# Performance work log

Measured on AMD Instinct MI355X. Metric: run time of the kernel, lower is better.

The kernel has to match this reference:

```python
import jax, jax.numpy as jnp
import numpy as np

K_SAMPLES = 1024   # number of farthest-point samples (self.K)
K_NEIGH = 64       # neighbors per ball (self.k_classes)
RADIUS = 0.2       # ball-query radius
LAYERS = [64, 64, 128]
IN_CH = 3


def _fps_indices(pts, k):
    """Iterative farthest point sampling (pytorch3d-style, start at index 0).
    pts: (B, N, D) -> idx: (B, k) int32."""
    B, N, D = pts.shape
    big = jnp.asarray(1e10, pts.dtype)

    def step(carry, _):
        min_d, last = carry                                   # (B,N), (B,)
        lp = jnp.take_along_axis(pts, last[:, None, None], axis=1)  # (B,1,D)
        d = jnp.sum((pts - lp) ** 2, axis=-1)                 # (B,N)
        min_d = jnp.minimum(min_d, d)
        nxt = jnp.argmax(min_d, axis=-1).astype(jnp.int32)    # farthest so far
        return (min_d, nxt), nxt

    init = (jnp.full((B, N), big, pts.dtype), jnp.zeros((B,), jnp.int32))
    _, rest = jax.lax.scan(step, init, None, length=k - 1)    # (k-1, B)
    idx = jnp.concatenate([jnp.zeros((1, B), jnp.int32), rest], axis=0)
    return idx.T                                              # (B, k)


def _ball_query(queries, pts, k, radius):
    """For each query take the first k points of pts within radius (by index
    order, as in pytorch3d.ball_query); pad missing neighbors with zeros.
    queries: (B,K,D), pts: (B,N,D) -> grouped: (B,K,k,D)."""
    B, N, D = pts.shape
    q2 = jnp.sum(queries ** 2, axis=-1)                       # (B,K)
    p2 = jnp.sum(pts ** 2, axis=-1)                           # (B,N)
    d2 = q2[:, :, None] + p2[:, None, :] - 2.0 * jnp.einsum('bkd,bnd->bkn', queries, pts)
    valid = d2 < radius * radius                              # (B,K,N)
    arange_n = jnp.arange(N, dtype=jnp.int32)
    key = jnp.where(valid, arange_n, N)                       # invalid -> sentinel N
    neg_vals, nbr_idx = jax.lax.top_k(-key, k)                # k smallest keys
    taken_valid = (-neg_vals) < N                             # (B,K,k)
    grouped = jax.vmap(lambda p, i: p[i])(pts, nbr_idx)       # (B,K,k,D)
    grouped = jnp.where(taken_valid[..., None], grouped, jnp.zeros((), pts.dtype))
    return grouped


def setup_inputs() -> dict:
    key = jax.random.key(0)
    ks = jax.random.split(key, 7)
    points = jax.random.uniform(ks[0], (8, 4096, IN_CH), dtype=jnp.float32)
    dims = [IN_CH] + LAYERS
    inp = {'points': points}
    for li in range(len(LAYERS)):
        fan_in = dims[li]
        w = jax.random.normal(ks[1 + li], (dims[li], dims[li + 1]), dtype=jnp.float32) / np.sqrt(fan_in)
        b = jnp.zeros((dims[li + 1],), jnp.float32)
        inp[f'w{li}'] = w
        inp[f'b{li}'] = b
    return inp


def reference(points, w0, b0, w1, b1, w2, b2):
    # 1) farthest point sampling of K centroids
    fps_idx = _fps_indices(points, K_SAMPLES)                 # (B,K)
    selected = jax.vmap(lambda p, i: p[i])(points, fps_idx)   # (B,K,C)
    selected_xyz = selected[:, :, :3]
    # 2) ball query grouping around the centroids
    grouped = _ball_query(selected, points, K_NEIGH, RADIUS)  # (B,K,k,C)
    # 3) shared PointNet MLP (pointwise 1x1 conv == linear) + max-pool over neighbors
    h = grouped
    for w, b in ((w0, b0), (w1, b1), (w2, b2)):
        h = jax.nn.relu(jnp.einsum('bknc,cd->bknd', h, w) + b)
    feat = jnp.max(h, axis=2)                                 # (B,K,layers[-1])
    # 4) concat centroid xyz with pooled features
    return jnp.concatenate([selected_xyz, feat], axis=2)      # (B,K,3+128)
```

## Files before the change

kernel.cpp:

```cpp
#include <hip/hip_runtime.h>

#define BATCH 8
#define NPTS 4096
#define KSAMP 1024
#define KNEI 64
#define OUTC 131

__device__ __forceinline__ unsigned long long umax64(unsigned long long a,
                                                     unsigned long long b)
{
    return a > b ? a : b;
}

#define DPP_U64_STEP(v, CTRL)                                                  \
    {                                                                          \
        int _lo = __builtin_amdgcn_update_dpp(0, (int)(unsigned)(v), (CTRL),   \
                                              0xF, 0xF, true);                 \
        int _hi = __builtin_amdgcn_update_dpp(0, (int)((v) >> 32), (CTRL),     \
                                              0xF, 0xF, true);                 \
        unsigned long long _o =                                                \
            ((unsigned long long)(unsigned)_hi << 32) | (unsigned)_lo;         \
        (v) = umax64((v), _o);                                                 \
    }

__device__ __forceinline__ unsigned long long wave_umax64(unsigned long long v)
{
    DPP_U64_STEP(v, 0x111)
    DPP_U64_STEP(v, 0x112)
    DPP_U64_STEP(v, 0x114)
    DPP_U64_STEP(v, 0x118)
    DPP_U64_STEP(v, 0x142)
    DPP_U64_STEP(v, 0x143)
    return v;
}

#define DPP_F32MAX_STEP(v, CTRL)                                               \
    {                                                                          \
        int _s = __builtin_amdgcn_update_dpp(0, __float_as_int(v), (CTRL),     \
                                             0xF, 0xF, true);                  \
        (v) = fmaxf((v), __int_as_float(_s));                                  \
    }

__device__ __forceinline__ float wave_fmax_nonneg(float v)
{
    DPP_F32MAX_STEP(v, 0x111)
    DPP_F32MAX_STEP(v, 0x112)
    DPP_F32MAX_STEP(v, 0x114)
    DPP_F32MAX_STEP(v, 0x118)
    DPP_F32MAX_STEP(v, 0x142)
    DPP_F32MAX_STEP(v, 0x143)
    return v;
}

#define FPS_T 256
#define FPS_PPT 16

__global__ __launch_bounds__(FPS_T) void fps_kernel(const float* __restrict__ pts,
                                                    float* __restrict__ out)
{
    const int b = blockIdx.x;
    const int t = threadIdx.x;
    const float* p = pts + (size_t)b * NPTS * 3;

    __shared__ float lx[NPTS], ly[NPTS], lz[NPTS];
    __shared__ unsigned long long cand[2][4];

    float px[FPS_PPT], py[FPS_PPT], pz[FPS_PPT], md[FPS_PPT];
#pragma unroll
    for (int i = 0; i < FPS_PPT; ++i) {
        const int n = t * FPS_PPT + i;
        px[i] = p[n * 3 + 0];
        py[i] = p[n * 3 + 1];
        pz[i] = p[n * 3 + 2];
        lx[n] = px[i]; ly[n] = py[i]; lz[n] = pz[i];
        md[i] = 1e10f;
    }
    if (t == 0) {
        float* o = out + (size_t)b * KSAMP * OUTC;
        o[0] = p[0]; o[1] = p[1]; o[2] = p[2];
    }
    __syncthreads();

    const int wave = t >> 6;
    const int lane = t & 63;
    int cur = 0;

    for (int s = 1; s < KSAMP; ++s) {
        const float qx = lx[cur], qy = ly[cur], qz = lz[cur];

#pragma unroll
        for (int i = 0; i < FPS_PPT; ++i) {
            float dx = px[i] - qx, dy = py[i] - qy, dz = pz[i] - qz;
            float d = dx * dx + dy * dy + dz * dz;
            md[i] = fminf(md[i], d);
        }

        unsigned long long c[FPS_PPT];
#pragma unroll
        for (int i = 0; i < FPS_PPT; ++i)
            c[i] = ((unsigned long long)__float_as_uint(md[i]) << 32)
                 | (unsigned)(4095 - (t * FPS_PPT + i));
#pragma unroll
        for (int i = 0; i < 8; ++i) c[i] = umax64(c[i], c[i + 8]);
#pragma unroll
        for (int i = 0; i < 4; ++i) c[i] = umax64(c[i], c[i + 4]);
        c[0] = umax64(c[0], c[2]);
        c[1] = umax64(c[1], c[3]);
        unsigned long long best = umax64(c[0], c[1]);

        best = wave_umax64(best);
        const int par = s & 1;
        if (lane == 63) cand[par][wave] = best;
        __syncthreads();

        unsigned long long g = umax64(umax64(cand[par][0], cand[par][1]),
                                      umax64(cand[par][2], cand[par][3]));
        cur = 4095 - (int)(g & 0xffffffffu);

        if (t == 0) {
            float* o = out + ((size_t)b * KSAMP + s) * OUTC;
            o[0] = lx[cur]; o[1] = ly[cur]; o[2] = lz[cur];
        }
    }
}

__global__ __launch_bounds__(64) void bqmlp_kernel(
    const float* __restrict__ pts,
    const float* __restrict__ w0, const float* __restrict__ b0,
    const float* __restrict__ w1, const float* __restrict__ b1,
    const float* __restrict__ w2, const float* __restrict__ b2,
    float* __restrict__ out)
{
    const int q    = blockIdx.x;
    const int b    = q >> 10;
    const int lane = threadIdx.x;
    const float* p = pts + (size_t)b * NPTS * 3;
    float* orow    = out + (size_t)q * OUTC;

    const float qx = orow[0], qy = orow[1], qz = orow[2];

    const float RR = 0.04f;
    const float q2 = __fadd_rn(__fadd_rn(__fmul_rn(qx, qx), __fmul_rn(qy, qy)),
                               __fmul_rn(qz, qz));

    __shared__ float nx[KNEI], ny[KNEI], nz[KNEI];
    nx[lane] = 0.0f; ny[lane] = 0.0f; nz[lane] = 0.0f;
    __syncthreads();

    int total = 0;
    for (int c = 0; c < NPTS / 64 && total < KNEI; ++c) {
        const int n = c * 64 + lane;
        const float x = p[n * 3 + 0];
        const float y = p[n * 3 + 1];
        const float z = p[n * 3 + 2];
        const float p2  = __fadd_rn(__fadd_rn(__fmul_rn(x, x), __fmul_rn(y, y)),
                                    __fmul_rn(z, z));
        const float dot = __fadd_rn(__fadd_rn(__fmul_rn(qx, x), __fmul_rn(qy, y)),
                                    __fmul_rn(qz, z));
        const float d2  = __fsub_rn(__fadd_rn(q2, p2), __fmul_rn(2.0f, dot));
        const bool valid = d2 < RR;
        const unsigned long long mask = __ballot(valid);
        const int pos = total + (int)__popcll(mask & ((1ull << lane) - 1ull));
        if (valid && pos < KNEI) { nx[pos] = x; ny[pos] = y; nz[pos] = z; }
        total += (int)__popcll(mask);
    }
    __syncthreads();

    const float x = nx[lane], y = ny[lane], z = nz[lane];

    float h0[64];
#pragma unroll
    for (int j = 0; j < 64; ++j) {
        float a = fmaf(x, w0[j], fmaf(y, w0[64 + j], fmaf(z, w0[128 + j], b0[j])));
        h0[j] = fmaxf(a, 0.0f);
    }

    float h1[64];
#pragma unroll
    for (int jb = 0; jb < 4; ++jb) {
        float acc[16];
#pragma unroll
        for (int i = 0; i < 16; ++i) acc[i] = b1[jb * 16 + i];
#pragma unroll
        for (int k = 0; k < 64; ++k) {
#pragma unroll
            for (int i = 0; i < 16; ++i)
                acc[i] = fmaf(h0[k], w1[k * 64 + jb * 16 + i], acc[i]);
        }
#pragma unroll
        for (int i = 0; i < 16; ++i) h1[jb * 16 + i] = fmaxf(acc[i], 0.0f);
    }

#pragma unroll
    for (int jb = 0; jb < 8; ++jb) {
        float acc[16];
#pragma unroll
        for (int i = 0; i < 16; ++i) acc[i] = b2[jb * 16 + i];
#pragma unroll
        for (int k = 0; k < 64; ++k) {
#pragma unroll
            for (int i = 0; i < 16; ++i)
                acc[i] = fmaf(h1[k], w2[k * 128 + jb * 16 + i], acc[i]);
        }
#pragma unroll
        for (int i = 0; i < 16; ++i) {
            float v = fmaxf(acc[i], 0.0f);
            acc[i] = wave_fmax_nonneg(v);
        }
        if (lane == 63) {
#pragma unroll
            for (int i = 0; i < 16; ++i) orow[3 + jb * 16 + i] = acc[i];
        }
    }
}

extern "C" void kernel_launch(void* const* d_in, const int* in_sizes, int n_in,
                              void* d_out, int out_size, void* d_ws, size_t ws_size,
                              hipStream_t stream)
{
    (void)in_sizes; (void)n_in; (void)out_size; (void)d_ws; (void)ws_size;
    const float* pts = (const float*)d_in[0];
    const float* w0  = (const float*)d_in[1];
    const float* b0  = (const float*)d_in[2];
    const float* w1  = (const float*)d_in[3];
    const float* b1  = (const float*)d_in[4];
    const float* w2  = (const float*)d_in[5];
    const float* b2  = (const float*)d_in[6];
    float* out = (float*)d_out;

    hipLaunchKernelGGL(fps_kernel, dim3(BATCH), dim3(FPS_T), 0, stream, pts, out);
    hipLaunchKernelGGL(bqmlp_kernel, dim3(BATCH * KSAMP), dim3(64), 0, stream,
                       pts, w0, b0, w1, b1, w2, b2, out);
}
```

Baseline: 974.1 us.

## Pack FPS distance math, use index-tracked argmax, stage MLP weights in LDS

The FPS loop now computes distances with packed v_pk FP32 instructions and runs its per-thread argmax as float compares with index selects, building only one 64-bit key before the wave reduction. It also loads the next query point right after the reduction. The ball-query/MLP kernel now runs four queries per 256-thread block and stages all weights and biases in LDS as float4, in place of scalar global loads per lane. The LDS cost is about 50KB per block, which may limit occupancy, and staging adds a block-wide barrier.

```diff
diff --git a/kernel.cpp b/kernel.cpp
--- a/kernel.cpp
+++ b/kernel.cpp
@@ -5,6 +5,19 @@
 #define KSAMP 1024
 #define KNEI 64
 #define OUTC 131
+
+typedef float v2f __attribute__((ext_vector_type(2)));
+typedef float v4f __attribute__((ext_vector_type(4)));
+
+__device__ __forceinline__ v2f pk_add(v2f a, v2f b) {
+    v2f d; asm("v_pk_add_f32 %0, %1, %2" : "=v"(d) : "v"(a), "v"(b)); return d;
+}
+__device__ __forceinline__ v2f pk_mul(v2f a, v2f b) {
+    v2f d; asm("v_pk_mul_f32 %0, %1, %2" : "=v"(d) : "v"(a), "v"(b)); return d;
+}
+__device__ __forceinline__ v2f pk_fma(v2f a, v2f b, v2f c) {
+    v2f d; asm("v_pk_fma_f32 %0, %1, %2, %3" : "=v"(d) : "v"(a), "v"(b), "v"(c)); return d;
+}
 
 __device__ __forceinline__ unsigned long long umax64(unsigned long long a,
                                                      unsigned long long b)
@@ -65,15 +78,20 @@
     __shared__ float lx[NPTS], ly[NPTS], lz[NPTS];
     __shared__ unsigned long long cand[2][4];
 
-    float px[FPS_PPT], py[FPS_PPT], pz[FPS_PPT], md[FPS_PPT];
+    v2f pxp[8], pyp[8], pzp[8], mdp[8];
+    int idxr[16];
 #pragma unroll
     for (int i = 0; i < FPS_PPT; ++i) {
         const int n = t * FPS_PPT + i;
-        px[i] = p[n * 3 + 0];
-        py[i] = p[n * 3 + 1];
-        pz[i] = p[n * 3 + 2];
-        lx[n] = px[i]; ly[n] = py[i]; lz[n] = pz[i];
-        md[i] = 1e10f;
+        const float x = p[n * 3 + 0];
+        const float y = p[n * 3 + 1];
+        const float z = p[n * 3 + 2];
+        pxp[i >> 1][i & 1] = x;
+        pyp[i >> 1][i & 1] = y;
+        pzp[i >> 1][i & 1] = z;
+        mdp[i >> 1][i & 1] = 1e10f;
+        lx[n] = x; ly[n] = y; lz[n] = z;
+        idxr[i] = n;
     }
     if (t == 0) {
         float* o = out + (size_t)b * KSAMP * OUTC;
@@ -83,69 +101,111 @@
 
     const int wave = t >> 6;
     const int lane = t & 63;
-    int cur = 0;
+    float qx = lx[0], qy = ly[0], qz = lz[0];
+
+#define MD(i) ((i) & 1 ? mdp[(i) >> 1].y : mdp[(i) >> 1].x)
 
     for (int s = 1; s < KSAMP; ++s) {
-        const float qx = lx[cur], qy = ly[cur], qz = lz[cur];
-
-#pragma unroll
-        for (int i = 0; i < FPS_PPT; ++i) {
-            float dx = px[i] - qx, dy = py[i] - qy, dz = pz[i] - qz;
-            float d = dx * dx + dy * dy + dz * dz;
-            md[i] = fminf(md[i], d);
-        }
-
-        unsigned long long c[FPS_PPT];
-#pragma unroll
-        for (int i = 0; i < FPS_PPT; ++i)
-            c[i] = ((unsigned long long)__float_as_uint(md[i]) << 32)
-                 | (unsigned)(4095 - (t * FPS_PPT + i));
-#pragma unroll
-        for (int i = 0; i < 8; ++i) c[i] = umax64(c[i], c[i + 8]);
-#pragma unroll
-        for (int i = 0; i < 4; ++i) c[i] = umax64(c[i], c[i + 4]);
-        c[0] = umax64(c[0], c[2]);
-        c[1] = umax64(c[1], c[3]);
-        unsigned long long best = umax64(c[0], c[1]);
-
-        best = wave_umax64(best);
+        const float nqx = -qx, nqy = -qy, nqz = -qz;
+        const v2f nqx2 = {nqx, nqx}, nqy2 = {nqy, nqy}, nqz2 = {nqz, nqz};
+
+#pragma unroll
+        for (int j = 0; j < 8; ++j) {
+            v2f dx = pk_add(pxp[j], nqx2);
+            v2f dy = pk_add(pyp[j], nqy2);
+            v2f dz = pk_add(pzp[j], nqz2);
+            v2f d  = pk_fma(dz, dz, pk_fma(dy, dy, pk_mul(dx, dx)));
+            mdp[j].x = fminf(mdp[j].x, d.x);
+            mdp[j].y = fminf(mdp[j].y, d.y);
+        }
+
+        float tv[8]; int ti[8];
+#pragma unroll
+        for (int i = 0; i < 8; ++i) {
+            const float a = MD(i), c = MD(i + 8);
+            const bool g = c > a;
+            tv[i] = g ? c : a;
+            ti[i] = g ? idxr[i + 8] : idxr[i];
+        }
+#pragma unroll
+        for (int i = 0; i < 4; ++i) {
+            const bool g = tv[i + 4] > tv[i];
+            tv[i] = g ? tv[i + 4] : tv[i];
+            ti[i] = g ? ti[i + 4] : ti[i];
+        }
+#pragma unroll
+        for (int i = 0; i < 2; ++i) {
+            const bool g = tv[i + 2] > tv[i];
+            tv[i] = g ? tv[i + 2] : tv[i];
+            ti[i] = g ? ti[i + 2] : ti[i];
+        }
+        const bool g0 = tv[1] > tv[0];
+        const float bv = g0 ? tv[1] : tv[0];
+        const int   bi = g0 ? ti[1] : ti[0];
+
+        unsigned long long key =
+            ((unsigned long long)__float_as_uint(bv) << 32) | (unsigned)(4095 - bi);
+        key = wave_umax64(key);
         const int par = s & 1;
-        if (lane == 63) cand[par][wave] = best;
+        if (lane == 63) cand[par][wave] = key;
         __syncthreads();
 
-        unsigned long long g = umax64(umax64(cand[par][0], cand[par][1]),
-                                      umax64(cand[par][2], cand[par][3]));
-        cur = 4095 - (int)(g & 0xffffffffu);
-
+        const unsigned long long g =
+            umax64(umax64(cand[par][0], cand[par][1]),
+                   umax64(cand[par][2], cand[par][3]));
+        const int cur = 4095 - (int)(g & 0xffffffffu);
+
+        qx = lx[cur]; qy = ly[cur]; qz = lz[cur];
         if (t == 0) {
             float* o = out + ((size_t)b * KSAMP + s) * OUTC;
-            o[0] = lx[cur]; o[1] = ly[cur]; o[2] = lz[cur];
-        }
-    }
-}
-
-__global__ __launch_bounds__(64) void bqmlp_kernel(
+            o[0] = qx; o[1] = qy; o[2] = qz;
+        }
+    }
+#undef MD
+}
+
+__global__ __launch_bounds__(256, 3) void bqmlp_kernel(
     const float* __restrict__ pts,
     const float* __restrict__ w0, const float* __restrict__ b0,
     const float* __restrict__ w1, const float* __restrict__ b1,
     const float* __restrict__ w2, const float* __restrict__ b2,
     float* __restrict__ out)
 {
-    const int q    = blockIdx.x;
-    const int b    = q >> 10;
-    const int lane = threadIdx.x;
-    const float* p = pts + (size_t)b * NPTS * 3;
+    const int t    = threadIdx.x;
+    const int wv   = t >> 6;
+    const int lane = t & 63;
+    const int q    = blockIdx.x * 4 + wv;
+    const int bb   = q >> 10;
+    const float* p = pts + (size_t)bb * NPTS * 3;
     float* orow    = out + (size_t)q * OUTC;
 
+    __shared__ v4f sw0[48];
+    __shared__ v4f sb0[16];
+    __shared__ v4f sw1[1024];
+    __shared__ v4f sb1[16];
+    __shared__ v4f sw2[2048];
+    __shared__ v4f sb2[32];
+    __shared__ float snx[4][KNEI], sny[4][KNEI], snz[4][KNEI];
+
+    {
+        const v4f* g1 = (const v4f*)w1;
+#pragma unroll
+        for (int i = 0; i < 4; ++i) sw1[t + i * 256] = g1[t + i * 256];
+        const v4f* g2 = (const v4f*)w2;
+#pragma unroll
+        for (int i = 0; i < 8; ++i) sw2[t + i * 256] = g2[t + i * 256];
+        if (t < 48) sw0[t] = ((const v4f*)w0)[t];
+        if (t < 16) sb0[t] = ((const v4f*)b0)[t];
+        if (t < 16) sb1[t] = ((const v4f*)b1)[t];
+        if (t < 32) sb2[t] = ((const v4f*)b2)[t];
+    }
+
     const float qx = orow[0], qy = orow[1], qz = orow[2];
-
     const float RR = 0.04f;
     const float q2 = __fadd_rn(__fadd_rn(__fmul_rn(qx, qx), __fmul_rn(qy, qy)),
                                __fmul_rn(qz, qz));
 
-    __shared__ float nx[KNEI], ny[KNEI], nz[KNEI];
-    nx[lane] = 0.0f; ny[lane] = 0.0f; nz[lane] = 0.0f;
-    __syncthreads();
+    snx[wv][lane] = 0.0f; sny[wv][lane] = 0.0f; snz[wv][lane] = 0.0f;
 
     int total = 0;
     for (int c = 0; c < NPTS / 64 && total < KNEI; ++c) {
@@ -161,18 +221,23 @@
         const bool valid = d2 < RR;
         const unsigned long long mask = __ballot(valid);
         const int pos = total + (int)__popcll(mask & ((1ull << lane) - 1ull));
-        if (valid && pos < KNEI) { nx[pos] = x; ny[pos] = y; nz[pos] = z; }
+        if (valid && pos < KNEI) { snx[wv][pos] = x; sny[wv][pos] = y; snz[wv][pos] = z; }
         total += (int)__popcll(mask);
     }
+
     __syncthreads();
 
-    const float x = nx[lane], y = ny[lane], z = nz[lane];
+    const float x = snx[wv][lane], y = sny[wv][lane], z = snz[wv][lane];
 
     float h0[64];
 #pragma unroll
-    for (int j = 0; j < 64; ++j) {
-        float a = fmaf(x, w0[j], fmaf(y, w0[64 + j], fmaf(z, w0[128 + j], b0[j])));
-        h0[j] = fmaxf(a, 0.0f);
+    for (int j4 = 0; j4 < 16; ++j4) {
+        const v4f wx = sw0[j4], wy = sw0[16 + j4], wz = sw0[32 + j4], bv = sb0[j4];
+#pragma unroll
+        for (int c = 0; c < 4; ++c) {
+            float a = fmaf(x, wx[c], fmaf(y, wy[c], fmaf(z, wz[c], bv[c])));
+            h0[j4 * 4 + c] = fmaxf(a, 0.0f);
+        }
     }
 
     float h1[64];
@@ -180,12 +245,25 @@
     for (int jb = 0; jb < 4; ++jb) {
         float acc[16];
 #pragma unroll
-        for (int i = 0; i < 16; ++i) acc[i] = b1[jb * 16 + i];
+        for (int i4 = 0; i4 < 4; ++i4) {
+            const v4f bv = sb1[jb * 4 + i4];
+#pragma unroll
+            for (int c = 0; c < 4; ++c) acc[i4 * 4 + c] = bv[c];
+        }
 #pragma unroll
         for (int k = 0; k < 64; ++k) {
-#pragma unroll
-            for (int i = 0; i < 16; ++i)
-                acc[i] = fmaf(h0[k], w1[k * 64 + jb * 16 + i], acc[i]);
+            const float hk = h0[k];
+            const v4f wA = sw1[k * 16 + jb * 4 + 0];
+            const v4f wB = sw1[k * 16 + jb * 4 + 1];
+            const v4f wC = sw1[k * 16 + jb * 4 + 2];
+            const v4f wD = sw1[k * 16 + jb * 4 + 3];
+#pragma unroll
+            for (int c = 0; c < 4; ++c) {
+                acc[c]      = fmaf(hk, wA[c], acc[c]);
+                acc[4 + c]  = fmaf(hk, wB[c], acc[4 + c]);
+                acc[8 + c]  = fmaf(hk, wC[c], acc[8 + c]);
+                acc[12 + c] = fmaf(hk, wD[c], acc[12 + c]);
+            }
         }
 #pragma unroll
         for (int i = 0; i < 16; ++i) h1[jb * 16 + i] = fmaxf(acc[i], 0.0f);
@@ -195,12 +273,25 @@
     for (int jb = 0; jb < 8; ++jb) {
         float acc[16];
 #pragma unroll
-        for (int i = 0; i < 16; ++i) acc[i] = b2[jb * 16 + i];
+        for (int i4 = 0; i4 < 4; ++i4) {
+            const v4f bv = sb2[jb * 4 + i4];
+#pragma unroll
+            for (int c = 0; c < 4; ++c) acc[i4 * 4 + c] = bv[c];
+        }
 #pragma unroll
         for (int k = 0; k < 64; ++k) {
-#pragma unroll
-            for (int i = 0; i < 16; ++i)
-                acc[i] = fmaf(h1[k], w2[k * 128 + jb * 16 + i], acc[i]);
+            const float hk = h1[k];
+            const v4f wA = sw2[k * 32 + jb * 4 + 0];
+            const v4f wB = sw2[k * 32 + jb * 4 + 1];
+            const v4f wC = sw2[k * 32 + jb * 4 + 2];
+            const v4f wD = sw2[k * 32 + jb * 4 + 3];
+#pragma unroll
+            for (int c = 0; c < 4; ++c) {
+                acc[c]      = fmaf(hk, wA[c], acc[c]);
+                acc[4 + c]  = fmaf(hk, wB[c], acc[4 + c]);
+                acc[8 + c]  = fmaf(hk, wC[c], acc[8 + c]);
+                acc[12 + c] = fmaf(hk, wD[c], acc[12 + c]);
+            }
         }
 #pragma unroll
         for (int i = 0; i < 16; ++i) {
@@ -229,6 +320,6 @@
     float* out = (float*)d_out;
 
     hipLaunchKernelGGL(fps_kernel, dim3(BATCH), dim3(FPS_T), 0, stream, pts, out);
-    hipLaunchKernelGGL(bqmlp_kernel, dim3(BATCH * KSAMP), dim3(64), 0, stream,
+    hipLaunchKernelGGL(bqmlp_kernel, dim3(BATCH * KSAMP / 4), dim3(256), 0, stream,
                        pts, w0, b0, w1, b1, w2, b2, out);
 }
```

Result: slower. 1.851 ms (+90.0%).

## Run MLP layers on bf16 MFMA with hi/lo split for fp32 accuracy

Applied to the files above, without the earlier changes.

Replaces the per-lane fp32 FMA chains for the 64x64 and 64x128 MLP layers with 16x16x32 bf16 MFMA instructions. Operands are split into high and low bf16 parts and combined with three MFMAs to approximate fp32 precision. A prep kernel pre-splits and repacks the weights into the workspace, and activations are staged through padded shared memory. This adds an extra launch and a dependence on workspace size, keeping the fp32 kernel as a fallback, and gives a small accuracy risk from dropping the lo*lo term.

```diff
diff --git a/kernel.cpp b/kernel.cpp
--- a/kernel.cpp
+++ b/kernel.cpp
@@ -5,6 +5,19 @@
 #define KSAMP 1024
 #define KNEI 64
 #define OUTC 131
+
+typedef __attribute__((ext_vector_type(8))) short  bf16x8;
+typedef __attribute__((ext_vector_type(4))) float  f32x4;
+
+__device__ __forceinline__ unsigned short f2bf_rne(float f)
+{
+    unsigned u = __float_as_uint(f);
+    return (unsigned short)((u + 0x7FFFu + ((u >> 16) & 1u)) >> 16);
+}
+__device__ __forceinline__ float bf2f(unsigned short h)
+{
+    return __uint_as_float(((unsigned)h) << 16);
+}
 
 __device__ __forceinline__ unsigned long long umax64(unsigned long long a,
                                                      unsigned long long b)
@@ -124,7 +137,208 @@
     }
 }
 
-__global__ __launch_bounds__(64) void bqmlp_kernel(
+__global__ __launch_bounds__(256) void prep_kernel(const float* __restrict__ w1,
+                                                   const float* __restrict__ w2,
+                                                   unsigned short* __restrict__ ws)
+{
+    const int tid = blockIdx.x * 256 + threadIdx.x;
+    if (tid >= 1536) return;
+    const int fid  = tid >> 6;
+    const int lane = tid & 63;
+    const int lg = lane >> 4, lr = lane & 15;
+
+    const float* W; int N, f; unsigned base_hi, base_lo;
+    if (fid < 8) { W = w1; N = 64;  f = fid;     base_hi = 0;    base_lo = 4096; }
+    else         { W = w2; N = 128; f = fid - 8; base_hi = 8192; base_lo = 16384; }
+    const int nt = f >> 1, kc = f & 1;
+    const int col = nt * 16 + lr;
+
+    bf16x8 hi8, lo8;
+#pragma unroll
+    for (int i = 0; i < 8; ++i) {
+        const int k = kc * 32 + lg * 8 + i;
+        const float w = W[k * N + col];
+        const unsigned short hs = f2bf_rne(w);
+        hi8[i] = (short)hs;
+        lo8[i] = (short)f2bf_rne(w - bf2f(hs));
+    }
+    ((bf16x8*)(ws + base_hi))[f * 64 + lane] = hi8;
+    ((bf16x8*)(ws + base_lo))[f * 64 + lane] = lo8;
+}
+
+#define HPAD 72
+
+__global__ __launch_bounds__(64) void bqmlp_mfma(
+    const float* __restrict__ pts,
+    const float* __restrict__ w0, const float* __restrict__ b0,
+    const float* __restrict__ b1, const float* __restrict__ b2,
+    const unsigned short* __restrict__ ws,
+    float* __restrict__ out)
+{
+    const int q    = blockIdx.x;
+    const int bb   = q >> 10;
+    const int lane = threadIdx.x;
+    const int lg   = lane >> 4, lr = lane & 15;
+    const float* p = pts + (size_t)bb * NPTS * 3;
+    float* orow    = out + (size_t)q * OUTC;
+
+    __shared__ unsigned short hb_hi[64 * HPAD];
+    __shared__ unsigned short hb_lo[64 * HPAD];
+    __shared__ float snx[KNEI], sny[KNEI], snz[KNEI];
+
+    const float qx = orow[0], qy = orow[1], qz = orow[2];
+    const float RR = 0.04f;
+    const float q2 = __fadd_rn(__fadd_rn(__fmul_rn(qx, qx), __fmul_rn(qy, qy)),
+                               __fmul_rn(qz, qz));
+
+    snx[lane] = 0.0f; sny[lane] = 0.0f; snz[lane] = 0.0f;
+    __syncthreads();
+
+    int total = 0;
+    for (int c = 0; c < NPTS / 64 && total < KNEI; ++c) {
+        const int n = c * 64 + lane;
+        const float x = p[n * 3 + 0];
+        const float y = p[n * 3 + 1];
+        const float z = p[n * 3 + 2];
+        const float p2  = __fadd_rn(__fadd_rn(__fmul_rn(x, x), __fmul_rn(y, y)),
+                                    __fmul_rn(z, z));
+        const float dot = __fadd_rn(__fadd_rn(__fmul_rn(qx, x), __fmul_rn(qy, y)),
+                                    __fmul_rn(qz, z));
+        const float d2  = __fsub_rn(__fadd_rn(q2, p2), __fmul_rn(2.0f, dot));
+        const bool valid = d2 < RR;
+        const unsigned long long mask = __ballot(valid);
+        const int pos = total + (int)__popcll(mask & ((1ull << lane) - 1ull));
+        if (valid && pos < KNEI) { snx[pos] = x; sny[pos] = y; snz[pos] = z; }
+        total += (int)__popcll(mask);
+    }
+    __syncthreads();
+
+    const float x = snx[lane], y = sny[lane], z = snz[lane];
+
+    float h0[64];
+#pragma unroll
+    for (int j = 0; j < 64; ++j) {
+        float a = fmaf(x, w0[j], fmaf(y, w0[64 + j], fmaf(z, w0[128 + j], b0[j])));
+        h0[j] = fmaxf(a, 0.0f);
+    }
+
+#pragma unroll
+    for (int c = 0; c < 8; ++c) {
+        bf16x8 hi8, lo8;
+#pragma unroll
+        for (int i = 0; i < 8; ++i) {
+            const float v = h0[c * 8 + i];
+            const unsigned short hs = f2bf_rne(v);
+            hi8[i] = (short)hs;
+            lo8[i] = (short)f2bf_rne(v - bf2f(hs));
+        }
+        *(bf16x8*)&hb_hi[lane * HPAD + c * 8] = hi8;
+        *(bf16x8*)&hb_lo[lane * HPAD + c * 8] = lo8;
+    }
+    __syncthreads();
+
+    const bf16x8* B1h = (const bf16x8*)ws;
+    const bf16x8* B1l = B1h + 512;
+    const bf16x8* B2h = B1h + 1024;
+    const bf16x8* B2l = B1h + 2048;
+
+    f32x4 acc2[4][4];
+#pragma unroll
+    for (int nt = 0; nt < 4; ++nt) {
+        const float bv = b1[nt * 16 + lr];
+#pragma unroll
+        for (int mt = 0; mt < 4; ++mt)
+            acc2[mt][nt] = (f32x4){bv, bv, bv, bv};
+    }
+
+#pragma unroll
+    for (int mt = 0; mt < 4; ++mt) {
+        bf16x8 ah[2], al[2];
+#pragma unroll
+        for (int kc = 0; kc < 2; ++kc) {
+            ah[kc] = *(const bf16x8*)&hb_hi[(mt * 16 + lr) * HPAD + kc * 32 + lg * 8];
+            al[kc] = *(const bf16x8*)&hb_lo[(mt * 16 + lr) * HPAD + kc * 32 + lg * 8];
+        }
+#pragma unroll
+        for (int nt = 0; nt < 4; ++nt) {
+#pragma unroll
+            for (int kc = 0; kc < 2; ++kc) {
+                const bf16x8 bh = B1h[(nt * 2 + kc) * 64 + lane];
+                const bf16x8 bl = B1l[(nt * 2 + kc) * 64 + lane];
+                acc2[mt][nt] = __builtin_amdgcn_mfma_f32_16x16x32_bf16(ah[kc], bh, acc2[mt][nt], 0, 0, 0);
+                acc2[mt][nt] = __builtin_amdgcn_mfma_f32_16x16x32_bf16(ah[kc], bl, acc2[mt][nt], 0, 0, 0);
+                acc2[mt][nt] = __builtin_amdgcn_mfma_f32_16x16x32_bf16(al[kc], bh, acc2[mt][nt], 0, 0, 0);
+            }
+        }
+    }
+
+    __syncthreads();
+#pragma unroll
+    for (int mt = 0; mt < 4; ++mt) {
+#pragma unroll
+        for (int nt = 0; nt < 4; ++nt) {
+#pragma unroll
+            for (int r = 0; r < 4; ++r) {
+                const float v = fmaxf(acc2[mt][nt][r], 0.0f);
+                const int row = mt * 16 + lg * 4 + r;
+                const int col = nt * 16 + lr;
+                const unsigned short hs = f2bf_rne(v);
+                hb_hi[row * HPAD + col] = hs;
+                hb_lo[row * HPAD + col] = f2bf_rne(v - bf2f(hs));
+            }
+        }
+    }
+    __syncthreads();
+
+#pragma unroll
+    for (int h = 0; h < 2; ++h) {
+        f32x4 acc3[4][4];
+#pragma unroll
+        for (int nt4 = 0; nt4 < 4; ++nt4) {
+            const float bv = b2[(h * 4 + nt4) * 16 + lr];
+#pragma unroll
+            for (int mt = 0; mt < 4; ++mt)
+                acc3[mt][nt4] = (f32x4){bv, bv, bv, bv};
+        }
+
+#pragma unroll
+        for (int mt = 0; mt < 4; ++mt) {
+            bf16x8 ah[2], al[2];
+#pragma unroll
+            for (int kc = 0; kc < 2; ++kc) {
+                ah[kc] = *(const bf16x8*)&hb_hi[(mt * 16 + lr) * HPAD + kc * 32 + lg * 8];
+                al[kc] = *(const bf16x8*)&hb_lo[(mt * 16 + lr) * HPAD + kc * 32 + lg * 8];
+            }
+#pragma unroll
+            for (int nt4 = 0; nt4 < 4; ++nt4) {
+                const int f = (h * 4 + nt4) * 2;
+#pragma unroll
+                for (int kc = 0; kc < 2; ++kc) {
+                    const bf16x8 bh = B2h[(f + kc) * 64 + lane];
+                    const bf16x8 bl = B2l[(f + kc) * 64 + lane];
+                    acc3[mt][nt4] = __builtin_amdgcn_mfma_f32_16x16x32_bf16(ah[kc], bh, acc3[mt][nt4], 0, 0, 0);
+                    acc3[mt][nt4] = __builtin_amdgcn_mfma_f32_16x16x32_bf16(ah[kc], bl, acc3[mt][nt4], 0, 0, 0);
+                    acc3[mt][nt4] = __builtin_amdgcn_mfma_f32_16x16x32_bf16(al[kc], bh, acc3[mt][nt4], 0, 0, 0);
+                }
+            }
+        }
+
+#pragma unroll
+        for (int nt4 = 0; nt4 < 4; ++nt4) {
+            float m = 0.0f;
+#pragma unroll
+            for (int mt = 0; mt < 4; ++mt)
+#pragma unroll
+                for (int r = 0; r < 4; ++r)
+                    m = fmaxf(m, acc3[mt][nt4][r]);
+            m = fmaxf(m, __shfl_xor(m, 16));
+            m = fmaxf(m, __shfl_xor(m, 32));
+            if (lane < 16) orow[3 + (h * 4 + nt4) * 16 + lane] = m;
+        }
+    }
+}
+
+__global__ __launch_bounds__(64) void bqmlp_fp32(
     const float* __restrict__ pts,
     const float* __restrict__ w0, const float* __restrict__ b0,
     const float* __restrict__ w1, const float* __restrict__ b1,
@@ -132,13 +346,12 @@
     float* __restrict__ out)
 {
     const int q    = blockIdx.x;
-    const int b    = q >> 10;
+    const int bb   = q >> 10;
     const int lane = threadIdx.x;
-    const float* p = pts + (size_t)b * NPTS * 3;
+    const float* p = pts + (size_t)bb * NPTS * 3;
     float* orow    = out + (size_t)q * OUTC;
 
     const float qx = orow[0], qy = orow[1], qz = orow[2];
-
     const float RR = 0.04f;
     const float q2 = __fadd_rn(__fadd_rn(__fmul_rn(qx, qx), __fmul_rn(qy, qy)),
                                __fmul_rn(qz, qz));
@@ -218,7 +431,7 @@
                               void* d_out, int out_size, void* d_ws, size_t ws_size,
                               hipStream_t stream)
 {
-    (void)in_sizes; (void)n_in; (void)out_size; (void)d_ws; (void)ws_size;
+    (void)in_sizes; (void)n_in; (void)out_size;
     const float* pts = (const float*)d_in[0];
     const float* w0  = (const float*)d_in[1];
     const float* b0  = (const float*)d_in[2];
@@ -229,6 +442,14 @@
     float* out = (float*)d_out;
 
     hipLaunchKernelGGL(fps_kernel, dim3(BATCH), dim3(FPS_T), 0, stream, pts, out);
-    hipLaunchKernelGGL(bqmlp_kernel, dim3(BATCH * KSAMP), dim3(64), 0, stream,
-                       pts, w0, b0, w1, b1, w2, b2, out);
-}
+
+    if (ws_size >= 49152) {
+        unsigned short* wsp = (unsigned short*)d_ws;
+        hipLaunchKernelGGL(prep_kernel, dim3(6), dim3(256), 0, stream, w1, w2, wsp);
+        hipLaunchKernelGGL(bqmlp_mfma, dim3(BATCH * KSAMP), dim3(64), 0, stream,
+                           pts, w0, b0, b1, b2, wsp, out);
+    } else {
+        hipLaunchKernelGGL(bqmlp_fp32, dim3(BATCH * KSAMP), dim3(64), 0, stream,
+                           pts, w0, b0, w1, b1, w2, b2, out);
+    }
+}
```

Measured after the change: 793.4 us. -18.6%, faster.
